# Kernel tuning notes

Hardware: AMD Instinct MI355X
Metric: run time of the kernel (lower is better)

The kernel has to match this reference:

```python
import jax, jax.numpy as jnp
import numpy as np

STRIDE = 15           # cfg.shm.dilation_kernel
PAD = STRIDE // 2
P = 1048576           # cfg.shm.max_n_pixel (static sparse-pixel budget)


def dilate(alpha):
    # mask = (0.01 < alpha < 0.99); then 15x15 max-pool, stride 1, pad 7 (same size)
    m = jnp.logical_and(alpha > 0.01, alpha < 0.99).astype(alpha.dtype)
    return jax.lax.reduce_window(
        m, -jnp.inf, jax.lax.max,
        (1, 1, STRIDE, STRIDE), (1, 1, 1, 1),
        [(0, 0), (0, 0), (PAD, PAD), (PAD, PAD)])


def setup_inputs() -> dict:
    key = jax.random.key(0)
    ks = jax.random.split(key, 8)
    d = 128
    return {
        'image': jax.random.normal(ks[0], (8, 3, 512, 512), jnp.float32),
        'lr_pred': jax.random.uniform(ks[1], (8, 1, 512, 512), jnp.float32),
        'W1': jax.random.normal(ks[2], (4, d), jnp.float32) * 0.5,
        'b1': jnp.zeros((d,), jnp.float32),
        'W2': jax.random.normal(ks[3], (d, d), jnp.float32) * (1.0 / np.sqrt(d)),
        'b2': jnp.zeros((d,), jnp.float32),
        'W3': jax.random.normal(ks[4], (d, 1), jnp.float32) * (1.0 / np.sqrt(d)),
        'b3': jnp.zeros((1,), jnp.float32),
    }


def reference(image, lr_pred, W1, b1, W2, b2, W3, b3):
    B, C, H, W = image.shape
    mask = dilate(lr_pred)                       # [B,1,H,W] dilated uncertainty mask

    # generate_sparse_inputs: cat(img, (lr_pred-0.5)/0.5) channels-last, gather where mask>0
    feat = jnp.concatenate([image, (lr_pred - 0.5) / 0.5], axis=1)  # [B,4,H,W]
    feat = feat.transpose(0, 2, 3, 1).reshape(-1, C + 1)            # [B*H*W, 4]
    mflat = mask.reshape(-1)                                        # [B*H*W]

    (idx,) = jnp.nonzero(mflat > 0, size=P, fill_value=0)           # static-size gather
    count = jnp.sum(mflat > 0)
    valid = (jnp.arange(P) < count).astype(feat.dtype)              # [P]

    # torch's generate_sparse_inputs runs under no_grad -> stop_gradient on gather
    x = jax.lax.stop_gradient(feat[idx])                            # [P,4]

    # stand-in sparse head (shm): per-pixel MLP with sigmoid alpha output
    h = jax.nn.relu(x @ W1 + b1)
    h = jax.nn.relu(h @ W2 + b2)
    pred = jax.nn.sigmoid(h @ W3 + b3)[:, 0]                        # [P]

    # scatter predictions back to dense grid; ungathered masked pixels keep lr_pred
    scattered = jnp.zeros_like(mflat).at[idx].add(pred * valid)
    covered = jnp.zeros_like(mflat).at[idx].add(valid)
    lrf = lr_pred.reshape(-1)
    dense = scattered + (1.0 - covered) * lrf

    # final blend: pred*mask + lr_pred*(1-mask)
    final = dense * mflat + lrf * (1.0 - mflat)
    return final.reshape(B, 1, H, W)
```

## Files before the change

### kernel.cpp

```cpp
#include <hip/hip_runtime.h>
#include <hip/hip_bf16.h>
#include <math.h>

#define BB 8
#define HH 512
#define WW 512
#define NPIX (BB * HH * WW)
#define HWPIX (HH * WW)
#define PBUD 1048576
#define RAD 7
#define NB (NPIX / 256)
#define NMLP (NPIX / 128)

typedef __attribute__((ext_vector_type(4))) float f32x4;
typedef __attribute__((ext_vector_type(8))) short short8;
typedef __attribute__((ext_vector_type(4))) unsigned int u32x4;

__device__ __forceinline__ unsigned short f2bf(float f) {
    unsigned int u = __float_as_uint(f);
    unsigned int r = (u + 0x7fffu + ((u >> 16) & 1u)) >> 16;
    return (unsigned short)r;
}

__device__ __forceinline__ unsigned int pkbf(float a, float b) {
    __hip_bfloat162 h = __float22bfloat162_rn(make_float2(a, b));
    return *(unsigned int*)&h;
}

__global__ void k_prep_w2(const float* __restrict__ w2, unsigned short* __restrict__ w2f) {
    int i = blockIdx.x * 256 + threadIdx.x;
    int e  = i & 7;
    int l  = (i >> 3) & 63;
    int ks = (i >> 9) & 3;
    int jc = i >> 11;
    int j = jc * 16 + (l & 15);
    int k = ks * 32 + ((l >> 4) & 3) * 8 + e;
    w2f[i] = f2bf(w2[k * 128 + j]);
}

__global__ void k_rowdil(const float* __restrict__ lr, unsigned char* __restrict__ rowdil) {
    int p = blockIdx.x * 256 + threadIdx.x;
    int w = p & (WW - 1);
    int row0 = p - w;
    int lo = w - RAD; if (lo < 0) lo = 0;
    int hi = w + RAD; if (hi > WW - 1) hi = WW - 1;
    unsigned char any = 0;
    for (int x = lo; x <= hi; ++x) {
        float v = lr[row0 + x];
        any |= (unsigned char)(v > 0.01f && v < 0.99f);
    }
    rowdil[p] = any;
}

__global__ void k_coldil(const unsigned char* __restrict__ rowdil,
                         unsigned char* __restrict__ dm,
                         unsigned char* __restrict__ rankb,
                         int* __restrict__ gsum) {
    int p = blockIdx.x * 256 + threadIdx.x;
    int h = (p >> 9) & (HH - 1);
    int lo = h - RAD; if (lo < 0) lo = 0;
    int hi = h + RAD; if (hi > HH - 1) hi = HH - 1;
    lo -= h; hi -= h;
    unsigned char any = 0;
    for (int d = lo; d <= hi; ++d) any |= rowdil[p + d * WW];
    dm[p] = any;

    unsigned long long bal = __ballot(any != 0);
    __shared__ int wsum[4];
    int lane = threadIdx.x & 63;
    int wid  = threadIdx.x >> 6;
    if (lane == 0) wsum[wid] = __popcll(bal);
    __syncthreads();
    int pre = __popcll(bal & ((1ull << lane) - 1ull));
    int woff = 0;
    for (int i = 0; i < wid; ++i) woff += wsum[i];
    rankb[p] = (unsigned char)(woff + pre);
    if (threadIdx.x == 0) gsum[blockIdx.x] = wsum[0] + wsum[1] + wsum[2] + wsum[3];
}

__global__ void k_scan(const int* __restrict__ gsum, int* __restrict__ goff) {
    __shared__ int tsum[1024];
    int t = threadIdx.x;
    int base = t * 8;
    int v[8];
    int s = 0;
#pragma unroll
    for (int i = 0; i < 8; ++i) { v[i] = gsum[base + i]; s += v[i]; }
    tsum[t] = s;
    __syncthreads();
    for (int off = 1; off < 1024; off <<= 1) {
        int x = tsum[t];
        int y = (t >= off) ? tsum[t - off] : 0;
        __syncthreads();
        tsum[t] = x + y;
        __syncthreads();
    }
    int run = (t == 0) ? 0 : tsum[t - 1];
#pragma unroll
    for (int i = 0; i < 8; ++i) { goff[base + i] = run; run += v[i]; }
}

__global__ __launch_bounds__(256, 4)
void k_mlp(const float* __restrict__ image, const float* __restrict__ lr,
           const float* __restrict__ w1, const float* __restrict__ b1,
           const unsigned short* __restrict__ w2f, const float* __restrict__ b2,
           const float* __restrict__ w3, const float* __restrict__ b3,
           const unsigned char* __restrict__ dm, const unsigned char* __restrict__ rankb,
           const int* __restrict__ goff, float* __restrict__ out) {
    __shared__ __align__(16) char lds[32768];
    __shared__ int s_any;
    int g  = blockIdx.x;
    int p0 = g * 128;
    int t  = threadIdx.x;

    if (t == 0) s_any = 0;
    __syncthreads();
    if (t < 128) {
        int p = p0 + t;
        if (dm[p] && (goff[p >> 8] + (int)rankb[p] < PBUD)) s_any = 1;
    }
    __syncthreads();
    if (!s_any) {
        if (t < 128) out[p0 + t] = lr[p0 + t];
        return;
    }

    {
        int px = t & 127;
        int jh = __builtin_amdgcn_readfirstlane(t >> 7);
        int p  = p0 + px;
        float lrv = lr[p];
        size_t bimg = (size_t)(p >> 18) * 3 * HWPIX + (p & (HWPIX - 1));
        float x0 = image[bimg];
        float x1 = image[bimg + HWPIX];
        float x2 = image[bimg + 2 * HWPIX];
        float x3 = 2.0f * lrv - 1.0f;
#pragma unroll
        for (int jc8 = 0; jc8 < 8; ++jc8) {
            int jc = jh * 8 + jc8;
            float h[8];
#pragma unroll
            for (int e = 0; e < 8; ++e) {
                int j = jc * 8 + e;
                float a = b1[j];
                a = fmaf(x0, w1[j], a);
                a = fmaf(x1, w1[128 + j], a);
                a = fmaf(x2, w1[256 + j], a);
                a = fmaf(x3, w1[384 + j], a);
                h[e] = fmaxf(a, 0.0f);
            }
            u32x4 pk = { pkbf(h[0], h[1]), pkbf(h[2], h[3]),
                         pkbf(h[4], h[5]), pkbf(h[6], h[7]) };
            int a = (((px << 8) | (jc << 4))) ^ ((px & 15) << 4);
            *(u32x4*)(lds + a) = pk;
        }
    }
    __syncthreads();

    int w    = t >> 6;
    int l    = t & 63;
    int lr16 = l & 15;
    int lh   = l >> 4;
    int rowbase = w * 32;

    short8 af[2][4];
#pragma unroll
    for (int ks = 0; ks < 4; ++ks) {
#pragma unroll
        for (int mt = 0; mt < 2; ++mt) {
            int row = rowbase + mt * 16 + lr16;
            int a = (((row << 8) | (ks << 6) | (lh << 4))) ^ ((row & 15) << 4);
            af[mt][ks] = *(const short8*)(lds + a);
        }
    }

    float b2v[8], w3v[8];
#pragma unroll
    for (int jc = 0; jc < 8; ++jc) {
        int col = jc * 16 + lr16;
        b2v[jc] = b2[col];
        w3v[jc] = w3[col];
    }
    float b3v = b3[0];

    f32x4 acc[2][8];
#pragma unroll
    for (int mt = 0; mt < 2; ++mt)
#pragma unroll
        for (int jc = 0; jc < 8; ++jc)
            acc[mt][jc] = (f32x4){b2v[jc], b2v[jc], b2v[jc], b2v[jc]};

    const short8* wf = (const short8*)w2f;
#pragma unroll
    for (int jc = 0; jc < 8; ++jc) {
        short8 bf[4];
#pragma unroll
        for (int ks = 0; ks < 4; ++ks) bf[ks] = wf[(jc * 4 + ks) * 64 + l];
#pragma unroll
        for (int ks = 0; ks < 4; ++ks) {
            acc[0][jc] = __builtin_amdgcn_mfma_f32_16x16x32_bf16(af[0][ks], bf[ks], acc[0][jc], 0, 0, 0);
            acc[1][jc] = __builtin_amdgcn_mfma_f32_16x16x32_bf16(af[1][ks], bf[ks], acc[1][jc], 0, 0, 0);
        }
    }

#pragma unroll
    for (int mt = 0; mt < 2; ++mt) {
#pragma unroll
        for (int r = 0; r < 4; ++r) {
            int row = rowbase + mt * 16 + lh * 4 + r;
            float part = 0.f;
#pragma unroll
            for (int jc = 0; jc < 8; ++jc)
                part += fmaxf(acc[mt][jc][r], 0.f) * w3v[jc];
            part += __shfl_xor(part, 1);
            part += __shfl_xor(part, 2);
            part += __shfl_xor(part, 4);
            part += __shfl_xor(part, 8);
            if (lr16 == 0) {
                int p = p0 + row;
                float lrv = lr[p];
                bool s = dm[p] && (goff[p >> 8] + (int)rankb[p] < PBUD);
                float logit = b3v + part;
                out[p] = s ? (1.0f / (1.0f + __expf(-logit))) : lrv;
            }
        }
    }
}

extern "C" void kernel_launch(void* const* d_in, const int* in_sizes, int n_in,
                              void* d_out, int out_size, void* d_ws, size_t ws_size,
                              hipStream_t stream) {
    const float* image = (const float*)d_in[0];
    const float* lr    = (const float*)d_in[1];
    const float* w1    = (const float*)d_in[2];
    const float* b1    = (const float*)d_in[3];
    const float* w2    = (const float*)d_in[4];
    const float* b2    = (const float*)d_in[5];
    const float* w3    = (const float*)d_in[6];
    const float* b3    = (const float*)d_in[7];
    float* out = (float*)d_out;

    char* ws = (char*)d_ws;
    unsigned char* rowdil = (unsigned char*)ws;
    unsigned char* dm     = (unsigned char*)(ws + (size_t)NPIX);
    unsigned char* rankb  = (unsigned char*)(ws + 2 * (size_t)NPIX);
    int* gsum             = (int*)(ws + 3 * (size_t)NPIX);
    int* goff             = (int*)(ws + 3 * (size_t)NPIX + NB * 4);
    unsigned short* w2f   = (unsigned short*)(ws + 3 * (size_t)NPIX + 2 * NB * 4);

    k_prep_w2<<<64, 256, 0, stream>>>(w2, w2f);
    k_rowdil <<<NPIX / 256, 256, 0, stream>>>(lr, rowdil);
    k_coldil <<<NB, 256, 0, stream>>>(rowdil, dm, rankb, gsum);
    k_scan   <<<1, 1024, 0, stream>>>(gsum, goff);
    k_mlp    <<<NMLP, 256, 0, stream>>>(image, lr, w1, b1, w2f, b2, w3, b3,
                                        dm, rankb, goff, out);
}
```

Measured before the change: 135.8 us.

## Split MLP second layer by output columns per wave, reduce partials via LDS

Each wave now owns 32 output columns of W2 across all 128 pixel rows instead of 32 rows across all columns, so its W2 fragments are loaded once into registers and reused over eight row tiles. Partial third-layer dot products are written to a small LDS array and summed across the four waves before the sigmoid. The mask and lr loads are hoisted so each thread reads them once, and the final store becomes a coalesced write by 128 threads instead of scattered single-lane stores. This lowers register pressure and repeated global W2 reads, at the cost of an extra barrier and more LDS A-fragment reads per wave.

```diff
diff --git a/kernel.cpp b/kernel.cpp
--- a/kernel.cpp
+++ b/kernel.cpp
@@ -108,28 +108,47 @@
            const unsigned char* __restrict__ dm, const unsigned char* __restrict__ rankb,
            const int* __restrict__ goff, float* __restrict__ out) {
     __shared__ __align__(16) char lds[32768];
+    __shared__ float part_l[4][128];
     __shared__ int s_any;
     int g  = blockIdx.x;
     int p0 = g * 128;
     int t  = threadIdx.x;
+    int px = t & 127;
+    int p  = p0 + px;
 
     if (t == 0) s_any = 0;
     __syncthreads();
-    if (t < 128) {
-        int p = p0 + t;
-        if (dm[p] && (goff[p >> 8] + (int)rankb[p] < PBUD)) s_any = 1;
-    }
+    float lrv = lr[p];
+    bool  sel = dm[p] && (goff[p >> 8] + (int)rankb[p] < PBUD);
+    if (sel) s_any = 1;
     __syncthreads();
     if (!s_any) {
-        if (t < 128) out[p0 + t] = lr[p0 + t];
+        if (t < 128) out[p] = lrv;
         return;
     }
 
+    int w    = t >> 6;
+    int l    = t & 63;
+    int lr16 = l & 15;
+    int lh   = l >> 4;
+
+    const short8* wf = (const short8*)w2f;
+    short8 bf[2][4];
+#pragma unroll
+    for (int jj = 0; jj < 2; ++jj)
+#pragma unroll
+        for (int ks = 0; ks < 4; ++ks)
+            bf[jj][ks] = wf[((2 * w + jj) * 4 + ks) * 64 + l];
+    float b2v[2], w3v[2];
+#pragma unroll
+    for (int jj = 0; jj < 2; ++jj) {
+        b2v[jj] = b2[(2 * w + jj) * 16 + lr16];
+        w3v[jj] = w3[(2 * w + jj) * 16 + lr16];
+    }
+    float b3v = b3[0];
+
     {
-        int px = t & 127;
         int jh = __builtin_amdgcn_readfirstlane(t >> 7);
-        int p  = p0 + px;
-        float lrv = lr[p];
         size_t bimg = (size_t)(p >> 18) * 3 * HWPIX + (p & (HWPIX - 1));
         float x0 = image[bimg];
         float x1 = image[bimg + HWPIX];
@@ -157,73 +176,37 @@
     }
     __syncthreads();
 
-    int w    = t >> 6;
-    int l    = t & 63;
-    int lr16 = l & 15;
-    int lh   = l >> 4;
-    int rowbase = w * 32;
-
-    short8 af[2][4];
-#pragma unroll
-    for (int ks = 0; ks < 4; ++ks) {
-#pragma unroll
-        for (int mt = 0; mt < 2; ++mt) {
-            int row = rowbase + mt * 16 + lr16;
+#pragma unroll
+    for (int mt = 0; mt < 8; ++mt) {
+        short8 af[4];
+#pragma unroll
+        for (int ks = 0; ks < 4; ++ks) {
+            int row = mt * 16 + lr16;
             int a = (((row << 8) | (ks << 6) | (lh << 4))) ^ ((row & 15) << 4);
-            af[mt][ks] = *(const short8*)(lds + a);
-        }
-    }
-
-    float b2v[8], w3v[8];
-#pragma unroll
-    for (int jc = 0; jc < 8; ++jc) {
-        int col = jc * 16 + lr16;
-        b2v[jc] = b2[col];
-        w3v[jc] = w3[col];
-    }
-    float b3v = b3[0];
-
-    f32x4 acc[2][8];
-#pragma unroll
-    for (int mt = 0; mt < 2; ++mt)
-#pragma unroll
-        for (int jc = 0; jc < 8; ++jc)
-            acc[mt][jc] = (f32x4){b2v[jc], b2v[jc], b2v[jc], b2v[jc]};
-
-    const short8* wf = (const short8*)w2f;
-#pragma unroll
-    for (int jc = 0; jc < 8; ++jc) {
-        short8 bf[4];
-#pragma unroll
-        for (int ks = 0; ks < 4; ++ks) bf[ks] = wf[(jc * 4 + ks) * 64 + l];
+            af[ks] = *(const short8*)(lds + a);
+        }
+        f32x4 a0 = (f32x4){b2v[0], b2v[0], b2v[0], b2v[0]};
+        f32x4 a1 = (f32x4){b2v[1], b2v[1], b2v[1], b2v[1]};
 #pragma unroll
         for (int ks = 0; ks < 4; ++ks) {
-            acc[0][jc] = __builtin_amdgcn_mfma_f32_16x16x32_bf16(af[0][ks], bf[ks], acc[0][jc], 0, 0, 0);
-            acc[1][jc] = __builtin_amdgcn_mfma_f32_16x16x32_bf16(af[1][ks], bf[ks], acc[1][jc], 0, 0, 0);
-        }
-    }
-
-#pragma unroll
-    for (int mt = 0; mt < 2; ++mt) {
+            a0 = __builtin_amdgcn_mfma_f32_16x16x32_bf16(af[ks], bf[0][ks], a0, 0, 0, 0);
+            a1 = __builtin_amdgcn_mfma_f32_16x16x32_bf16(af[ks], bf[1][ks], a1, 0, 0, 0);
+        }
 #pragma unroll
         for (int r = 0; r < 4; ++r) {
-            int row = rowbase + mt * 16 + lh * 4 + r;
-            float part = 0.f;
-#pragma unroll
-            for (int jc = 0; jc < 8; ++jc)
-                part += fmaxf(acc[mt][jc][r], 0.f) * w3v[jc];
+            float part = fmaxf(a0[r], 0.f) * w3v[0] + fmaxf(a1[r], 0.f) * w3v[1];
             part += __shfl_xor(part, 1);
             part += __shfl_xor(part, 2);
             part += __shfl_xor(part, 4);
             part += __shfl_xor(part, 8);
-            if (lr16 == 0) {
-                int p = p0 + row;
-                float lrv = lr[p];
-                bool s = dm[p] && (goff[p >> 8] + (int)rankb[p] < PBUD);
-                float logit = b3v + part;
-                out[p] = s ? (1.0f / (1.0f + __expf(-logit))) : lrv;
-            }
-        }
+            if (lr16 == 0) part_l[w][mt * 16 + lh * 4 + r] = part;
+        }
+    }
+    __syncthreads();
+
+    if (t < 128) {
+        float s = b3v + part_l[0][t] + part_l[1][t] + part_l[2][t] + part_l[3][t];
+        out[p] = sel ? (1.0f / (1.0f + __expf(-s))) : lrv;
     }
 }
 
```

New measurement: 132.5 us, median of 2. -2.4%, faster.

## Compact active pixel blocks into a worklist and process two halves per MLP block

Applied to the files above, without the earlier changes.

The scan kernel now also builds a compacted list of 256-pixel blocks that contain masked pixels within budget, and a separate vectorized copy kernel writes lr_pred to the output for every pixel. The MLP kernel is launched over all blocks but exits early unless its index falls in the active list; it handles 256 pixels as two 128-pixel halves and overlaps the first-layer computation of the second half with the MFMA work of the first half. This avoids scheduling and flag-checking work for inactive tiles, at the cost of an extra full-output copy pass, a second scan in a single-block kernel, and lower occupancy (launch bounds 256,2).

```diff
diff --git a/kernel.cpp b/kernel.cpp
--- a/kernel.cpp
+++ b/kernel.cpp
@@ -10,9 +10,9 @@
 #define PBUD 1048576
 #define RAD 7
 #define NB (NPIX / 256)
-#define NMLP (NPIX / 128)
 
 typedef __attribute__((ext_vector_type(4))) float f32x4;
+typedef __attribute__((ext_vector_type(4))) float float4v;
 typedef __attribute__((ext_vector_type(8))) short short8;
 typedef __attribute__((ext_vector_type(4))) unsigned int u32x4;
 
@@ -78,7 +78,8 @@
     if (threadIdx.x == 0) gsum[blockIdx.x] = wsum[0] + wsum[1] + wsum[2] + wsum[3];
 }
 
-__global__ void k_scan(const int* __restrict__ gsum, int* __restrict__ goff) {
+__global__ void k_scan(const int* __restrict__ gsum, int* __restrict__ goff,
+                       int* __restrict__ act, int* __restrict__ act_n) {
     __shared__ int tsum[1024];
     int t = threadIdx.x;
     int base = t * 8;
@@ -96,39 +97,71 @@
         __syncthreads();
     }
     int run = (t == 0) ? 0 : tsum[t - 1];
-#pragma unroll
-    for (int i = 0; i < 8; ++i) { goff[base + i] = run; run += v[i]; }
-}
-
-__global__ __launch_bounds__(256, 4)
-void k_mlp(const float* __restrict__ image, const float* __restrict__ lr,
-           const float* __restrict__ w1, const float* __restrict__ b1,
-           const unsigned short* __restrict__ w2f, const float* __restrict__ b2,
-           const float* __restrict__ w3, const float* __restrict__ b3,
-           const unsigned char* __restrict__ dm, const unsigned char* __restrict__ rankb,
-           const int* __restrict__ goff, float* __restrict__ out) {
+    int aflag[8];
+    int acnt = 0;
+#pragma unroll
+    for (int i = 0; i < 8; ++i) {
+        goff[base + i] = run;
+        aflag[i] = (v[i] > 0 && run < PBUD) ? 1 : 0;
+        acnt += aflag[i];
+        run += v[i];
+    }
+    __syncthreads();
+    tsum[t] = acnt;
+    __syncthreads();
+    for (int off = 1; off < 1024; off <<= 1) {
+        int x = tsum[t];
+        int y = (t >= off) ? tsum[t - off] : 0;
+        __syncthreads();
+        tsum[t] = x + y;
+        __syncthreads();
+    }
+    int aoff = tsum[t] - acnt;
+    if (t == 1023) act_n[0] = tsum[1023];
+#pragma unroll
+    for (int i = 0; i < 8; ++i)
+        if (aflag[i]) act[aoff++] = base + i;
+}
+
+__global__ void k_copy(const float* __restrict__ lr, float* __restrict__ out) {
+    int i = (blockIdx.x * 256 + threadIdx.x) * 4;
+    *(float4v*)(out + i) = *(const float4v*)(lr + i);
+}
+
+__global__ __launch_bounds__(256, 2)
+void k_mlp2(const float* __restrict__ image, const float* __restrict__ lr,
+            const float* __restrict__ w1, const float* __restrict__ b1,
+            const unsigned short* __restrict__ w2f, const float* __restrict__ b2,
+            const float* __restrict__ w3, const float* __restrict__ b3,
+            const unsigned char* __restrict__ dm, const unsigned char* __restrict__ rankb,
+            const int* __restrict__ goff, const int* __restrict__ act,
+            const int* __restrict__ act_n, float* __restrict__ out) {
+    int ab = blockIdx.x;
+    if (ab >= act_n[0]) return;
+    int p0A = act[ab] * 256;
+    int p0B = p0A + 128;
+
     __shared__ __align__(16) char lds[32768];
-    __shared__ int s_any;
-    int g  = blockIdx.x;
-    int p0 = g * 128;
-    int t  = threadIdx.x;
-
-    if (t == 0) s_any = 0;
-    __syncthreads();
-    if (t < 128) {
-        int p = p0 + t;
-        if (dm[p] && (goff[p >> 8] + (int)rankb[p] < PBUD)) s_any = 1;
-    }
-    __syncthreads();
-    if (!s_any) {
-        if (t < 128) out[p0 + t] = lr[p0 + t];
-        return;
-    }
+    int t    = threadIdx.x;
+    int w    = t >> 6;
+    int l    = t & 63;
+    int lr16 = l & 15;
+    int lh   = l >> 4;
+    int rowbase = w * 32;
+    int px   = t & 127;
+    int jh   = __builtin_amdgcn_readfirstlane(t >> 7);
+
+    float b2v[8], w3v[8];
+#pragma unroll
+    for (int jc = 0; jc < 8; ++jc) {
+        int col = jc * 16 + lr16;
+        b2v[jc] = b2[col];
+        w3v[jc] = w3[col];
+    }
+    float b3v = b3[0];
 
     {
-        int px = t & 127;
-        int jh = __builtin_amdgcn_readfirstlane(t >> 7);
-        int p  = p0 + px;
+        int p = p0A + px;
         float lrv = lr[p];
         size_t bimg = (size_t)(p >> 18) * 3 * HWPIX + (p & (HWPIX - 1));
         float x0 = image[bimg];
@@ -136,8 +169,8 @@
         float x2 = image[bimg + 2 * HWPIX];
         float x3 = 2.0f * lrv - 1.0f;
 #pragma unroll
-        for (int jc8 = 0; jc8 < 8; ++jc8) {
-            int jc = jh * 8 + jc8;
+        for (int k = 0; k < 8; ++k) {
+            int jc = jh * 8 + k;
             float h[8];
 #pragma unroll
             for (int e = 0; e < 8; ++e) {
@@ -157,31 +190,17 @@
     }
     __syncthreads();
 
-    int w    = t >> 6;
-    int l    = t & 63;
-    int lr16 = l & 15;
-    int lh   = l >> 4;
-    int rowbase = w * 32;
-
-    short8 af[2][4];
+    short8 afA[2][4];
 #pragma unroll
     for (int ks = 0; ks < 4; ++ks) {
 #pragma unroll
         for (int mt = 0; mt < 2; ++mt) {
             int row = rowbase + mt * 16 + lr16;
             int a = (((row << 8) | (ks << 6) | (lh << 4))) ^ ((row & 15) << 4);
-            af[mt][ks] = *(const short8*)(lds + a);
-        }
-    }
-
-    float b2v[8], w3v[8];
-#pragma unroll
-    for (int jc = 0; jc < 8; ++jc) {
-        int col = jc * 16 + lr16;
-        b2v[jc] = b2[col];
-        w3v[jc] = w3[col];
-    }
-    float b3v = b3[0];
+            afA[mt][ks] = *(const short8*)(lds + a);
+        }
+    }
+    __syncthreads();
 
     f32x4 acc[2][8];
 #pragma unroll
@@ -191,15 +210,44 @@
             acc[mt][jc] = (f32x4){b2v[jc], b2v[jc], b2v[jc], b2v[jc]};
 
     const short8* wf = (const short8*)w2f;
-#pragma unroll
-    for (int jc = 0; jc < 8; ++jc) {
-        short8 bf[4];
-#pragma unroll
-        for (int ks = 0; ks < 4; ++ks) bf[ks] = wf[(jc * 4 + ks) * 64 + l];
-#pragma unroll
-        for (int ks = 0; ks < 4; ++ks) {
-            acc[0][jc] = __builtin_amdgcn_mfma_f32_16x16x32_bf16(af[0][ks], bf[ks], acc[0][jc], 0, 0, 0);
-            acc[1][jc] = __builtin_amdgcn_mfma_f32_16x16x32_bf16(af[1][ks], bf[ks], acc[1][jc], 0, 0, 0);
+    {
+        int pB = p0B + px;
+        float lrvB = lr[pB];
+        size_t bimgB = (size_t)(pB >> 18) * 3 * HWPIX + (pB & (HWPIX - 1));
+        float y0 = image[bimgB];
+        float y1 = image[bimgB + HWPIX];
+        float y2 = image[bimgB + 2 * HWPIX];
+        float y3 = 2.0f * lrvB - 1.0f;
+#pragma unroll
+        for (int k = 0; k < 8; ++k) {
+            {
+                int jc = jh * 8 + k;
+                float h[8];
+#pragma unroll
+                for (int e = 0; e < 8; ++e) {
+                    int j = jc * 8 + e;
+                    float a = b1[j];
+                    a = fmaf(y0, w1[j], a);
+                    a = fmaf(y1, w1[128 + j], a);
+                    a = fmaf(y2, w1[256 + j], a);
+                    a = fmaf(y3, w1[384 + j], a);
+                    h[e] = fmaxf(a, 0.0f);
+                }
+                u32x4 pk = { pkbf(h[0], h[1]), pkbf(h[2], h[3]),
+                             pkbf(h[4], h[5]), pkbf(h[6], h[7]) };
+                int a = (((px << 8) | (jc << 4))) ^ ((px & 15) << 4);
+                *(u32x4*)(lds + a) = pk;
+            }
+            {
+                short8 bf[4];
+#pragma unroll
+                for (int ks = 0; ks < 4; ++ks) bf[ks] = wf[(k * 4 + ks) * 64 + l];
+#pragma unroll
+                for (int ks = 0; ks < 4; ++ks) {
+                    acc[0][k] = __builtin_amdgcn_mfma_f32_16x16x32_bf16(afA[0][ks], bf[ks], acc[0][k], 0, 0, 0);
+                    acc[1][k] = __builtin_amdgcn_mfma_f32_16x16x32_bf16(afA[1][ks], bf[ks], acc[1][k], 0, 0, 0);
+                }
+            }
         }
     }
 
@@ -217,11 +265,60 @@
             part += __shfl_xor(part, 4);
             part += __shfl_xor(part, 8);
             if (lr16 == 0) {
-                int p = p0 + row;
-                float lrv = lr[p];
-                bool s = dm[p] && (goff[p >> 8] + (int)rankb[p] < PBUD);
-                float logit = b3v + part;
-                out[p] = s ? (1.0f / (1.0f + __expf(-logit))) : lrv;
+                int pp = p0A + row;
+                bool ss = dm[pp] && (goff[pp >> 8] + (int)rankb[pp] < PBUD);
+                if (ss) out[pp] = 1.0f / (1.0f + __expf(-(b3v + part)));
+            }
+        }
+    }
+    __syncthreads();
+
+    short8 afB[2][4];
+#pragma unroll
+    for (int ks = 0; ks < 4; ++ks) {
+#pragma unroll
+        for (int mt = 0; mt < 2; ++mt) {
+            int row = rowbase + mt * 16 + lr16;
+            int a = (((row << 8) | (ks << 6) | (lh << 4))) ^ ((row & 15) << 4);
+            afB[mt][ks] = *(const short8*)(lds + a);
+        }
+    }
+
+#pragma unroll
+    for (int mt = 0; mt < 2; ++mt)
+#pragma unroll
+        for (int jc = 0; jc < 8; ++jc)
+            acc[mt][jc] = (f32x4){b2v[jc], b2v[jc], b2v[jc], b2v[jc]};
+
+#pragma unroll
+    for (int jc = 0; jc < 8; ++jc) {
+        short8 bf[4];
+#pragma unroll
+        for (int ks = 0; ks < 4; ++ks) bf[ks] = wf[(jc * 4 + ks) * 64 + l];
+#pragma unroll
+        for (int ks = 0; ks < 4; ++ks) {
+            acc[0][jc] = __builtin_amdgcn_mfma_f32_16x16x32_bf16(afB[0][ks], bf[ks], acc[0][jc], 0, 0, 0);
+            acc[1][jc] = __builtin_amdgcn_mfma_f32_16x16x32_bf16(afB[1][ks], bf[ks], acc[1][jc], 0, 0, 0);
+        }
+    }
+
+#pragma unroll
+    for (int mt = 0; mt < 2; ++mt) {
+#pragma unroll
+        for (int r = 0; r < 4; ++r) {
+            int row = rowbase + mt * 16 + lh * 4 + r;
+            float part = 0.f;
+#pragma unroll
+            for (int jc = 0; jc < 8; ++jc)
+                part += fmaxf(acc[mt][jc][r], 0.f) * w3v[jc];
+            part += __shfl_xor(part, 1);
+            part += __shfl_xor(part, 2);
+            part += __shfl_xor(part, 4);
+            part += __shfl_xor(part, 8);
+            if (lr16 == 0) {
+                int pp = p0B + row;
+                bool ss = dm[pp] && (goff[pp >> 8] + (int)rankb[pp] < PBUD);
+                if (ss) out[pp] = 1.0f / (1.0f + __expf(-(b3v + part)));
             }
         }
     }
@@ -246,12 +343,15 @@
     unsigned char* rankb  = (unsigned char*)(ws + 2 * (size_t)NPIX);
     int* gsum             = (int*)(ws + 3 * (size_t)NPIX);
     int* goff             = (int*)(ws + 3 * (size_t)NPIX + NB * 4);
-    unsigned short* w2f   = (unsigned short*)(ws + 3 * (size_t)NPIX + 2 * NB * 4);
+    int* act              = (int*)(ws + 3 * (size_t)NPIX + 2 * NB * 4);
+    int* act_n            = (int*)(ws + 3 * (size_t)NPIX + 3 * NB * 4);
+    unsigned short* w2f   = (unsigned short*)(ws + 3 * (size_t)NPIX + 3 * NB * 4 + 16);
 
     k_prep_w2<<<64, 256, 0, stream>>>(w2, w2f);
     k_rowdil <<<NPIX / 256, 256, 0, stream>>>(lr, rowdil);
     k_coldil <<<NB, 256, 0, stream>>>(rowdil, dm, rankb, gsum);
-    k_scan   <<<1, 1024, 0, stream>>>(gsum, goff);
-    k_mlp    <<<NMLP, 256, 0, stream>>>(image, lr, w1, b1, w2f, b2, w3, b3,
-                                        dm, rankb, goff, out);
-}
+    k_scan   <<<1, 1024, 0, stream>>>(gsum, goff, act, act_n);
+    k_copy   <<<NPIX / 1024, 256, 0, stream>>>(lr, out);
+    k_mlp2   <<<NB, 256, 0, stream>>>(image, lr, w1, b1, w2f, b2, w3, b3,
+                                      dm, rankb, goff, act, act_n, out);
+}
```

After: 206.7 us. 52.2% more time.
